# Optimization experiments

Hardware: AMD Instinct MI355X
Metric: run time of the kernel (lower is better)

The kernel has to match this reference:

```python
import jax, jax.numpy as jnp
import numpy as np

N = 50000
E = 800000
IN_DIM = 128
HID = 128
HEADS = 8
OUT_DIM = 64
LRELU_SLOPE = 0.2


def setup_inputs() -> dict:
    key = jax.random.key(0)
    ks = jax.random.split(key, 10)
    x = jax.random.normal(ks[0], (N, IN_DIM), dtype=jnp.float32)
    edge_index = jax.random.randint(ks[1], (2, E), 0, N, dtype=jnp.int64)
    c1 = HID // HEADS  # 16
    W1 = jax.random.normal(ks[2], (IN_DIM, HID), dtype=jnp.float32) * (1.0 / np.sqrt(IN_DIM))
    as1 = jax.random.normal(ks[3], (HEADS, c1), dtype=jnp.float32) * 0.1
    ad1 = jax.random.normal(ks[4], (HEADS, c1), dtype=jnp.float32) * 0.1
    b1 = jnp.zeros((HID,), dtype=jnp.float32)
    W2 = jax.random.normal(ks[5], (HID, OUT_DIM), dtype=jnp.float32) * (1.0 / np.sqrt(HID))
    as2 = jax.random.normal(ks[6], (1, OUT_DIM), dtype=jnp.float32) * 0.1
    ad2 = jax.random.normal(ks[7], (1, OUT_DIM), dtype=jnp.float32) * 0.1
    b2 = jnp.zeros((OUT_DIM,), dtype=jnp.float32)
    return {"x": x, "edge_index": edge_index, "W1": W1, "as1": as1, "ad1": ad1,
            "b1": b1, "W2": W2, "as2": as2, "ad2": ad2, "b2": b2}


def gat_conv(x, src, dst, W, a_src, a_dst, b, heads, ch, concat):
    n = x.shape[0]
    h = (x @ W).reshape(n, heads, ch)               # [N,H,C]
    alpha_s = jnp.sum(h * a_src, axis=-1)           # [N,H]
    alpha_d = jnp.sum(h * a_dst, axis=-1)           # [N,H]
    e = jax.nn.leaky_relu(alpha_s[src] + alpha_d[dst], LRELU_SLOPE)  # [E,H]
    m = jax.ops.segment_max(e, dst, num_segments=n)  # per-dst max (self-loops guarantee nonempty)
    e = jnp.exp(e - m[dst])
    denom = jax.ops.segment_sum(e, dst, num_segments=n)
    alpha = e / (denom[dst] + 1e-16)                # [E,H]
    msg = h[src] * alpha[:, :, None]                # [E,H,C]
    out = jax.ops.segment_sum(msg, dst, num_segments=n)  # [N,H,C]
    out = out.reshape(n, heads * ch) if concat else out.mean(axis=1)
    return out + b


def reference(x, edge_index, W1, as1, ad1, b1, W2, as2, ad2, b2):
    n = x.shape[0]
    loops = jnp.arange(n, dtype=edge_index.dtype)
    src = jnp.concatenate([edge_index[0], loops])   # PyG GATConv adds self-loops
    dst = jnp.concatenate([edge_index[1], loops])
    # layer 1: GATBlock (dropout is identity at eval), heads=8, concat, ELU
    h = gat_conv(x, src, dst, W1, as1, ad1, b1, HEADS, HID // HEADS, True)
    h = jax.nn.elu(h)
    # final conv: heads=1, concat=False
    out = gat_conv(h, src, dst, W2, as2, ad2, b2, 1, OUT_DIM, False)
    return jax.nn.log_softmax(out, axis=1)
```

## Files before the change

kernel.cpp:

```cpp
#include <hip/hip_runtime.h>
#include <hip/hip_bf16.h>
#include <math.h>

#define IN_DIM 128
#define HID 128
#define HEADS 8
#define OUT_DIM 64
#define SLOPE 0.2f
#define BSHIFT 7
#define BCAP 4096
#define BCAPSHIFT 12
#define EPT 8

typedef short bf16x8 __attribute__((ext_vector_type(8)));
typedef float f32x4 __attribute__((ext_vector_type(4)));

__device__ __forceinline__ float lrelu(float x) { return fmaxf(x, SLOPE * x); }
__device__ __forceinline__ float bf2f(unsigned u) { return __uint_as_float(u << 16); }
__device__ __forceinline__ unsigned short f2bf(float f) {
    unsigned u = __float_as_uint(f);
    return (unsigned short)((u + 0x7FFF + ((u >> 16) & 1)) >> 16);
}

__global__ __launch_bounds__(256) void setup_kernel(
    const float* __restrict__ W1, const float* __restrict__ W2,
    short* __restrict__ w1t, short* __restrict__ w2t, int* __restrict__ gcursor) {
    int t = threadIdx.x;
    int b = blockIdx.x;
    if (b == 96) {
        for (int i = t; i < 512; i += 256) gcursor[i] = 0;
        return;
    }
    if (b < 64) {
        int id = b * 256 + t;
        int n = id >> 7, k = id & 127;
        w1t[id] = (short)f2bf(W1[k * 128 + n]);
    } else {
        int id = (b - 64) * 256 + t;
        int n = id >> 7, k = id & 127;
        w2t[id] = (short)f2bf(W2[k * 64 + n]);
    }
}

__device__ __forceinline__ void bscatter_body(
    int blk, int* smem, const int* __restrict__ idx,
    int* __restrict__ gcursor, unsigned* __restrict__ bucket_buf,
    int E, int N, int NB) {
    int* hist  = smem;
    int* gbase = smem + 512;
    int* lbase = smem + 1024;
    int* wtot  = smem + 1536;
    int* misc  = smem + 1540;
    unsigned* sent = (unsigned*)(smem + 1552);
    unsigned* spos = (unsigned*)(smem + 3600);
    int t = threadIdx.x;
    for (int i = t; i < 512; i += 256) hist[i] = 0;
    if (t == 0) misc[1] = 0;
    __syncthreads();
    {
        int nz = (idx[2 * t + 1] != 0) + (idx[2 * t + 513] != 0);
        if (nz) atomicAdd(&misc[1], nz);
    }
    __syncthreads();
    int flag = (misc[1] > 16) ? 1 : 0;
    int e0 = blk * (256 * EPT);
    int EN = E + N;
    unsigned ent[EPT];
    int bid[EPT];
    int loc[EPT];
#pragma unroll
    for (int k = 0; k < EPT; k++) {
        int e = e0 + k * 256 + t;
        bid[k] = -1;
        if (e < EN) {
            int src, dst;
            if (e < E) {
                if (flag) { src = idx[e]; dst = idx[E + e]; }
                else      { src = idx[2 * e]; dst = idx[2 * (E + e)]; }
            } else {
                src = dst = e - E;
            }
            int b = dst >> BSHIFT;
            bid[k] = b;
            ent[k] = ((unsigned)(dst & ((1 << BSHIFT) - 1)) << 16) | (unsigned)src;
            loc[k] = atomicAdd(&hist[b], 1);
        }
    }
    __syncthreads();
    int i0 = 2 * t;
    int a = hist[i0], b2 = hist[i0 + 1];
    int ps = a + b2;
    int lane = t & 63, w = t >> 6;
    int incl = ps;
#pragma unroll
    for (int off = 1; off < 64; off <<= 1) {
        int u = __shfl_up(incl, off, 64);
        if (lane >= off) incl += u;
    }
    if (lane == 63) wtot[w] = incl;
    __syncthreads();
    int woff = 0;
    for (int k = 0; k < w; k++) woff += wtot[k];
    int ex0 = woff + incl - ps;
    lbase[i0] = ex0;
    lbase[i0 + 1] = ex0 + a;
    if (t == 255) misc[0] = woff + incl;
    for (int i = t; i < 512; i += 256) {
        int c = hist[i];
        gbase[i] = c ? atomicAdd(&gcursor[i], c) : 0;
    }
    __syncthreads();
#pragma unroll
    for (int k = 0; k < EPT; k++) {
        if (bid[k] >= 0) {
            int p = lbase[bid[k]] + loc[k];
            int pib = gbase[bid[k]] + loc[k];
            sent[p] = ent[k];
            spos[p] = (pib < BCAP) ? (((unsigned)bid[k] << BCAPSHIFT) | (unsigned)pib)
                                   : 0xFFFFFFFFu;
        }
    }
    __syncthreads();
    int tot = misc[0];
    for (int i = t; i < tot; i += 256) {
        unsigned sp = spos[i];
        if (sp != 0xFFFFFFFFu) bucket_buf[sp] = sent[i];
    }
}

__device__ __forceinline__ void gemm1_body(
    int blk, char* smemraw, const float* __restrict__ x, const short* __restrict__ w1t,
    const float* __restrict__ a_s, const float* __restrict__ a_d,
    unsigned short* __restrict__ h1g, unsigned short* __restrict__ asb,
    float* __restrict__ ad_n, int N) {
    short* Wt = (short*)smemraw;
    float* hT = (float*)smemraw;
    int t = threadIdx.x;
    const uint4* src = (const uint4*)w1t;
    for (int id = t; id < 128 * 16; id += 256) {
        int n = id >> 4, kg = id & 15;
        *(uint4*)&Wt[n * 128 + ((kg * 8) ^ ((n & 7) << 3))] = src[id];
    }
    __syncthreads();
    int wv = t >> 6, lane = t & 63;
    int m = lane & 15, q = lane >> 4;
    int row = blk * 64 + wv * 16 + m;
    f32x4 acc[8];
#pragma unroll
    for (int j = 0; j < 8; j++) acc[j] = (f32x4){0.f, 0.f, 0.f, 0.f};
    int msw = (m & 7) << 3;
#pragma unroll
    for (int k0 = 0; k0 < 128; k0 += 32) {
        bf16x8 a = {0, 0, 0, 0, 0, 0, 0, 0};
        if (row < N) {
            const float* xp = &x[(size_t)row * 128 + k0 + q * 8];
            float4 u0 = *(const float4*)xp;
            float4 u1 = *(const float4*)(xp + 4);
            a[0] = (short)f2bf(u0.x); a[1] = (short)f2bf(u0.y);
            a[2] = (short)f2bf(u0.z); a[3] = (short)f2bf(u0.w);
            a[4] = (short)f2bf(u1.x); a[5] = (short)f2bf(u1.y);
            a[6] = (short)f2bf(u1.z); a[7] = (short)f2bf(u1.w);
        }
#pragma unroll
        for (int j = 0; j < 8; j++) {
            bf16x8 b = *(const bf16x8*)&Wt[(j * 16 + m) * 128 + ((k0 + q * 8) ^ msw)];
            acc[j] = __builtin_amdgcn_mfma_f32_16x16x32_bf16(a, b, acc[j], 0, 0, 0);
        }
    }
    __syncthreads();
#pragma unroll
    for (int r = 0; r < 4; r++) {
        int rl = wv * 16 + q * 4 + r;
        int sw = ((rl >> 2) & 1) << 4;
        int rb = rl * 128;
#pragma unroll
        for (int j = 0; j < 8; j++)
            hT[rb + ((j * 16 + m) ^ sw)] = acc[j][r];
    }
    __syncthreads();
    int base = blk * 64;
    for (int id = t; id < 1024; id += 256) {
        int rl = id >> 4, c8 = (id & 15) * 8;
        int rg = base + rl;
        if (rg >= N) continue;
        int sw = ((rl >> 2) & 1) << 4;
        float4 u0 = *(const float4*)&hT[rl * 128 + (c8 ^ sw)];
        float4 u1 = *(const float4*)&hT[rl * 128 + ((c8 + 4) ^ sw)];
        uint4 ow;
        ow.x = (unsigned)f2bf(u0.x) | ((unsigned)f2bf(u0.y) << 16);
        ow.y = (unsigned)f2bf(u0.z) | ((unsigned)f2bf(u0.w) << 16);
        ow.z = (unsigned)f2bf(u1.x) | ((unsigned)f2bf(u1.y) << 16);
        ow.w = (unsigned)f2bf(u1.z) | ((unsigned)f2bf(u1.w) << 16);
        *(uint4*)&h1g[(size_t)rg * 128 + c8] = ow;
    }
    for (int it = t; it < 512; it += 256) {
        int rl = it >> 3, hd = it & 7;
        int rg = base + rl;
        int sw = ((rl >> 2) & 1) << 4;
        const float* ap = a_s + hd * 16;
        const float* dp = a_d + hd * 16;
        float s = 0.f, d = 0.f;
#pragma unroll
        for (int p = 0; p < 4; p++) {
            float4 u = *(const float4*)&hT[rl * 128 + ((hd * 16 + p * 4) ^ sw)];
            s += u.x * ap[p * 4] + u.y * ap[p * 4 + 1] + u.z * ap[p * 4 + 2] + u.w * ap[p * 4 + 3];
            d += u.x * dp[p * 4] + u.y * dp[p * 4 + 1] + u.z * dp[p * 4 + 2] + u.w * dp[p * 4 + 3];
        }
        if (rg < N) {
            asb[(size_t)base * 8 + it] = f2bf(s);
            ad_n[(size_t)base * 8 + it] = d;
        }
    }
}

__global__ __launch_bounds__(256) void k1_kernel(
    const int* __restrict__ idx, int* __restrict__ gcursor,
    unsigned* __restrict__ bucket_buf,
    const float* __restrict__ x, const short* __restrict__ w1t,
    const float* __restrict__ a_s, const float* __restrict__ a_d,
    unsigned short* __restrict__ h1g, unsigned short* __restrict__ asb,
    float* __restrict__ ad_n, int E, int N, int NB, int GS) {
    __shared__ long long smem[4096];
    if ((int)blockIdx.x < GS)
        bscatter_body(blockIdx.x, (int*)smem, idx, gcursor, bucket_buf, E, N, NB);
    else
        gemm1_body(blockIdx.x - GS, (char*)smem, x, w1t, a_s, a_d, h1g, asb, ad_n, N);
}

__device__ __forceinline__ void bsort_body(
    int b, const int* __restrict__ gcursor, const unsigned* __restrict__ bucket_buf,
    int* __restrict__ row_start, int* __restrict__ sorted_src, int N, int NB) {
    __shared__ int cnt[128];
    __shared__ int cur[128];
    __shared__ int red[4];
    __shared__ int s_w0;
    __shared__ int srt[BCAP];
    int t = threadIdx.x;
    if (t < 128) cnt[t] = 0;
    int partial = 0;
    for (int i = t; i < b; i += 256) partial += min(gcursor[i], BCAP);
#pragma unroll
    for (int msk = 32; msk > 0; msk >>= 1) partial += __shfl_xor(partial, msk, 64);
    if ((t & 63) == 0) red[t >> 6] = partial;
    __syncthreads();
    int bbase = red[0] + red[1] + red[2] + red[3];
    int c = min(gcursor[b], BCAP);
    const unsigned* buf = bucket_buf + ((size_t)b << BCAPSHIFT);
    for (int i = t; i < c; i += 256)
        atomicAdd(&cnt[(buf[i] >> 16) & 127], 1);
    __syncthreads();
    int v = (t < 128) ? cnt[t] : 0;
    int lane = t & 63;
    int incl = v;
#pragma unroll
    for (int off = 1; off < 64; off <<= 1) {
        int u = __shfl_up(incl, off, 64);
        if (lane >= off) incl += u;
    }
    if (t == 63) s_w0 = incl;
    __syncthreads();
    if (t < 128) {
        int excl = incl - v + ((t >= 64) ? s_w0 : 0);
        cur[t] = excl;
        int node = (b << BSHIFT) + t;
        if (node <= N) row_start[node] = bbase + excl;
    }
    __syncthreads();
    for (int i = t; i < c; i += 256) {
        unsigned e = buf[i];
        int lp = atomicAdd(&cur[(e >> 16) & 127], 1);
        srt[lp] = (int)(e & 0xFFFFu);
    }
    __syncthreads();
    for (int i = t; i < c; i += 256)
        sorted_src[bbase + i] = srt[i];
}

__global__ __launch_bounds__(256) void k2_kernel(
    const int* __restrict__ gcursor, const unsigned* __restrict__ bucket_buf,
    int* __restrict__ row_start, int* __restrict__ sorted_src,
    int N, int NB, int EN) {
    if (blockIdx.x == 0 && threadIdx.x < 16) sorted_src[EN + threadIdx.x] = 0;
    bsort_body(blockIdx.x, gcursor, bucket_buf, row_start, sorted_src, N, NB);
}

__global__ __launch_bounds__(256) void mid_kernel(
    const int* __restrict__ row_start, const int* __restrict__ sorted_src,
    const unsigned short* __restrict__ asb, const float* __restrict__ ad_n,
    const unsigned short* __restrict__ h1g, const float* __restrict__ b1,
    const short* __restrict__ w2t, const float* __restrict__ a_s2,
    const float* __restrict__ a_d2, unsigned short* __restrict__ h2g,
    float* __restrict__ as2n, float* __restrict__ ad2n, int N) {
    __shared__ short hA[64 * 128];
    __shared__ short Wt[64 * 136];
    int t = threadIdx.x;
    const uint4* srcw = (const uint4*)w2t;
    for (int id = t; id < 64 * 16; id += 256) {
        int n = id >> 4, kg = id & 15;
        *(uint4*)&Wt[n * 136 + kg * 8] = srcw[id];
    }
    int lane = t & 63;
    int g = lane >> 4, j = lane & 15;
    int base = blockIdx.x * 64;
    int grp16 = (t >> 6) * 4 + g;
    int e4 = j >> 2;
    int hh = (j & 3) * 2;
    int hd = j >> 1;
    int hsel = hd & 1;
    int wsrc = hd >> 1;
    for (int ni = 0; ni < 4; ni++) {
        int rowl = ni * 16 + grp16;
        int node = base + rowl;
        float acc[8];
#pragma unroll
        for (int k = 0; k < 8; k++) acc[k] = 0.f;
        float denom = 0.f;
        if (node < N) {
            float2 adp = *(const float2*)&ad_n[(size_t)node * 8 + hh];
            int beg = row_start[node], end = row_start[node + 1];
            for (int i = beg; i < end; i += 4) {
                int se = sorted_src[i + e4];
                unsigned au = *(const unsigned*)&asb[(size_t)se * 8 + hh];
                float w0 = __expf(lrelu(bf2f(au & 0xffffu) + adp.x));
                float w1 = __expf(lrelu(bf2f(au >> 16) + adp.y));
                bool val = (i + e4 < end);
                w0 = val ? w0 : 0.f;
                w1 = val ? w1 : 0.f;
#pragma unroll
                for (int e = 0; e < 4; e++) {
                    int sl = e * 4 + wsrc;
                    int sg = __shfl(se, sl, 16);
                    float wa = __shfl(w0, sl, 16);
                    float wb = __shfl(w1, sl, 16);
                    float wv = hsel ? wb : wa;
                    uint4 hv = *(const uint4*)&h1g[(size_t)sg * 128 + j * 8];
                    acc[0] += wv * bf2f(hv.x & 0xffffu);
                    acc[1] += wv * bf2f(hv.x >> 16);
                    acc[2] += wv * bf2f(hv.y & 0xffffu);
                    acc[3] += wv * bf2f(hv.y >> 16);
                    acc[4] += wv * bf2f(hv.z & 0xffffu);
                    acc[5] += wv * bf2f(hv.z >> 16);
                    acc[6] += wv * bf2f(hv.w & 0xffffu);
                    acc[7] += wv * bf2f(hv.w >> 16);
                    denom += wv;
                }
            }
        }
        float inv = 1.f / (denom + 1e-16f);
        int c0 = j * 8;
        unsigned ow[4];
#pragma unroll
        for (int p = 0; p < 4; p++) {
            float v0 = acc[2 * p] * inv + b1[c0 + 2 * p];
            float v1 = acc[2 * p + 1] * inv + b1[c0 + 2 * p + 1];
            v0 = (v0 > 0.f) ? v0 : (__expf(v0) - 1.f);
            v1 = (v1 > 0.f) ? v1 : (__expf(v1) - 1.f);
            ow[p] = (unsigned)f2bf(v0) | ((unsigned)f2bf(v1) << 16);
        }
        uint4 val = (node < N) ? make_uint4(ow[0], ow[1], ow[2], ow[3])
                               : make_uint4(0, 0, 0, 0);
        *(uint4*)&hA[rowl * 128 + ((j * 8) ^ ((rowl & 7) << 3))] = val;
    }
    __syncthreads();
    int wv = t >> 6;
    int m = lane & 15, q = lane >> 4;
    int rowl = wv * 16 + m;
    int rsw = (rowl & 7) << 3;
    f32x4 acc2[4];
#pragma unroll
    for (int j4 = 0; j4 < 4; j4++) acc2[j4] = (f32x4){0.f, 0.f, 0.f, 0.f};
#pragma unroll
    for (int k0 = 0; k0 < 128; k0 += 32) {
        bf16x8 a = *(const bf16x8*)&hA[rowl * 128 + ((k0 + q * 8) ^ rsw)];
#pragma unroll
        for (int j4 = 0; j4 < 4; j4++) {
            bf16x8 b = *(const bf16x8*)&Wt[(j4 * 16 + m) * 136 + k0 + q * 8];
            acc2[j4] = __builtin_amdgcn_mfma_f32_16x16x32_bf16(a, b, acc2[j4], 0, 0, 0);
        }
    }
    float asl[4], adl[4];
#pragma unroll
    for (int j4 = 0; j4 < 4; j4++) { asl[j4] = a_s2[j4 * 16 + m]; adl[j4] = a_d2[j4 * 16 + m]; }
    int rbase = base + wv * 16 + q * 4;
#pragma unroll
    for (int r = 0; r < 4; r++) {
        int rr = rbase + r;
        float s = 0.f, d = 0.f;
#pragma unroll
        for (int j4 = 0; j4 < 4; j4++) {
            s += acc2[j4][r] * asl[j4];
            d += acc2[j4][r] * adl[j4];
        }
#pragma unroll
        for (int msk = 8; msk > 0; msk >>= 1) {
            s += __shfl_xor(s, msk, 64);
            d += __shfl_xor(d, msk, 64);
        }
        if (rr < N) {
            if (m == 0) { as2n[rr] = s; ad2n[rr] = d; }
#pragma unroll
            for (int j4 = 0; j4 < 4; j4++)
                h2g[(size_t)rr * 64 + j4 * 16 + m] = f2bf(acc2[j4][r]);
        }
    }
}

__global__ __launch_bounds__(256) void agg2_kernel(
    const int* __restrict__ row_start, const int* __restrict__ sorted_src,
    const float* __restrict__ as_n, const float* __restrict__ ad_n,
    const unsigned short* __restrict__ h2g, const float* __restrict__ b2,
    float* __restrict__ out, int N) {
    int lane = threadIdx.x & 63;
    int g = lane >> 4, j = lane & 15;
    int node = blockIdx.x * 16 + (threadIdx.x >> 6) * 4 + g;
    if (node >= N) return;
    int e4 = j >> 2;
    float adv = ad_n[node];
    int beg = row_start[node], end = row_start[node + 1];
    float acc[4];
#pragma unroll
    for (int k = 0; k < 4; k++) acc[k] = 0.f;
    float denom = 0.f;
    for (int i = beg; i < end; i += 4) {
        int se = sorted_src[i + e4];
        float w = __expf(lrelu(as_n[se] + adv));
        w = (i + e4 < end) ? w : 0.f;
#pragma unroll
        for (int e = 0; e < 4; e++) {
            int sg = __shfl(se, e * 4, 16);
            float wvv = __shfl(w, e * 4, 16);
            uint2 hv = *(const uint2*)&h2g[(size_t)sg * 64 + j * 4];
            acc[0] += wvv * bf2f(hv.x & 0xffffu);
            acc[1] += wvv * bf2f(hv.x >> 16);
            acc[2] += wvv * bf2f(hv.y & 0xffffu);
            acc[3] += wvv * bf2f(hv.y >> 16);
            denom += wvv;
        }
    }
    float inv = 1.f / (denom + 1e-16f);
    int c0 = j * 4;
    float v[4];
#pragma unroll
    for (int k = 0; k < 4; k++) v[k] = acc[k] * inv + b2[c0 + k];
    float mx = fmaxf(fmaxf(v[0], v[1]), fmaxf(v[2], v[3]));
#pragma unroll
    for (int msk = 8; msk > 0; msk >>= 1) mx = fmaxf(mx, __shfl_xor(mx, msk, 64));
    float ex = __expf(v[0] - mx) + __expf(v[1] - mx) + __expf(v[2] - mx) + __expf(v[3] - mx);
#pragma unroll
    for (int msk = 8; msk > 0; msk >>= 1) ex += __shfl_xor(ex, msk, 64);
    float lse = mx + __logf(ex);
    *(float4*)&out[(size_t)node * 64 + c0] = make_float4(v[0] - lse, v[1] - lse, v[2] - lse, v[3] - lse);
}

extern "C" void kernel_launch(void* const* d_in, const int* in_sizes, int n_in,
                              void* d_out, int out_size, void* d_ws, size_t ws_size,
                              hipStream_t stream) {
    const float* x   = (const float*)d_in[0];
    const int*   idx = (const int*)d_in[1];
    const float* W1  = (const float*)d_in[2];
    const float* as1 = (const float*)d_in[3];
    const float* ad1 = (const float*)d_in[4];
    const float* b1  = (const float*)d_in[5];
    const float* W2  = (const float*)d_in[6];
    const float* as2 = (const float*)d_in[7];
    const float* ad2 = (const float*)d_in[8];
    const float* b2  = (const float*)d_in[9];
    float* out = (float*)d_out;

    const int N = in_sizes[0] / IN_DIM;
    const int E = in_sizes[1] / 2;
    const int EN = E + N;
    const int NB = (N + (1 << BSHIFT) - 1) >> BSHIFT;
    const int GS = (EN + 256 * EPT - 1) / (256 * EPT);
    const int T1 = (N + 63) / 64;

    unsigned short* h1g   = (unsigned short*)d_ws;
    unsigned short* h1act = h1g + (size_t)N * 128;
    unsigned short* h2g   = h1act + (size_t)N * 128;
    unsigned short* as1b  = (unsigned short*)(h2g + (size_t)N * 64);
    float* ad1n = (float*)(as1b + (size_t)N * 8) + (size_t)N * 4;
    float* as2n = ad1n + (size_t)N * 8;
    float* ad2n = as2n + (size_t)N;
    int* row_start  = (int*)(ad2n + (size_t)N);
    int* gcursor    = row_start + N + 1;
    unsigned* bucket_buf = (unsigned*)(gcursor + 512);
    int* sorted_src = (int*)(bucket_buf + ((size_t)NB << BCAPSHIFT));
    short* w1t = (short*)((((uintptr_t)(sorted_src + EN + 16)) + 15) & ~(uintptr_t)15);
    short* w2t = w1t + 128 * 128;
    (void)ws_size; (void)n_in; (void)out_size;

    setup_kernel<<<97, 256, 0, stream>>>(W1, W2, w1t, w2t, gcursor);
    k1_kernel<<<GS + T1, 256, 0, stream>>>(idx, gcursor, bucket_buf,
                                           x, w1t, as1, ad1, h1g, as1b, ad1n, E, N, NB, GS);
    k2_kernel<<<NB, 256, 0, stream>>>(gcursor, bucket_buf, row_start, sorted_src, N, NB, EN);
    mid_kernel<<<T1, 256, 0, stream>>>(row_start, sorted_src, as1b, ad1n, h1g, b1,
                                       w2t, as2, ad2, h2g, as2n, ad2n, N);
    agg2_kernel<<<(N + 15) / 16, 256, 0, stream>>>(row_start, sorted_src, as2n, ad2n, h2g, b2, out, N);
}
```

Measured before the change: 183.3 us.

## Halve mid_kernel nodes per block and split GEMM columns across waves

The fused layer-1 aggregation plus layer-2 projection kernel now handles 32 nodes per block instead of 64, doubling the grid. In the MFMA stage each wave computes one row tile of 16 and half of the 64 output columns. The two attention-logit partial sums per row are combined through shared memory after an extra barrier. The goal is more blocks for better occupancy and load balance across CUs during the irregular gather phase, at the cost of reloading W2 into LDS twice as often and an additional sync.

```diff
diff --git a/kernel.cpp b/kernel.cpp
--- a/kernel.cpp
+++ b/kernel.cpp
@@ -291,8 +291,10 @@
     const short* __restrict__ w2t, const float* __restrict__ a_s2,
     const float* __restrict__ a_d2, unsigned short* __restrict__ h2g,
     float* __restrict__ as2n, float* __restrict__ ad2n, int N) {
-    __shared__ short hA[64 * 128];
+    __shared__ short hA[32 * 128];
     __shared__ short Wt[64 * 136];
+    __shared__ float sP[2][32];
+    __shared__ float dP[2][32];
     int t = threadIdx.x;
     const uint4* srcw = (const uint4*)w2t;
     for (int id = t; id < 64 * 16; id += 256) {
@@ -301,14 +303,14 @@
     }
     int lane = t & 63;
     int g = lane >> 4, j = lane & 15;
-    int base = blockIdx.x * 64;
+    int base = blockIdx.x * 32;
     int grp16 = (t >> 6) * 4 + g;
     int e4 = j >> 2;
     int hh = (j & 3) * 2;
     int hd = j >> 1;
     int hsel = hd & 1;
     int wsrc = hd >> 1;
-    for (int ni = 0; ni < 4; ni++) {
+    for (int ni = 0; ni < 2; ni++) {
         int rowl = ni * 16 + grp16;
         int node = base + rowl;
         float acc[8];
@@ -363,33 +365,40 @@
     }
     __syncthreads();
     int wv = t >> 6;
+    int rt = wv & 1;
+    int cp = wv >> 1;
     int m = lane & 15, q = lane >> 4;
-    int rowl = wv * 16 + m;
+    int rowl = rt * 16 + m;
     int rsw = (rowl & 7) << 3;
-    f32x4 acc2[4];
-#pragma unroll
-    for (int j4 = 0; j4 < 4; j4++) acc2[j4] = (f32x4){0.f, 0.f, 0.f, 0.f};
+    f32x4 acc2[2];
+#pragma unroll
+    for (int jj = 0; jj < 2; jj++) acc2[jj] = (f32x4){0.f, 0.f, 0.f, 0.f};
 #pragma unroll
     for (int k0 = 0; k0 < 128; k0 += 32) {
         bf16x8 a = *(const bf16x8*)&hA[rowl * 128 + ((k0 + q * 8) ^ rsw)];
 #pragma unroll
-        for (int j4 = 0; j4 < 4; j4++) {
+        for (int jj = 0; jj < 2; jj++) {
+            int j4 = cp * 2 + jj;
             bf16x8 b = *(const bf16x8*)&Wt[(j4 * 16 + m) * 136 + k0 + q * 8];
-            acc2[j4] = __builtin_amdgcn_mfma_f32_16x16x32_bf16(a, b, acc2[j4], 0, 0, 0);
-        }
-    }
-    float asl[4], adl[4];
-#pragma unroll
-    for (int j4 = 0; j4 < 4; j4++) { asl[j4] = a_s2[j4 * 16 + m]; adl[j4] = a_d2[j4 * 16 + m]; }
-    int rbase = base + wv * 16 + q * 4;
+            acc2[jj] = __builtin_amdgcn_mfma_f32_16x16x32_bf16(a, b, acc2[jj], 0, 0, 0);
+        }
+    }
+    float asl[2], adl[2];
+#pragma unroll
+    for (int jj = 0; jj < 2; jj++) {
+        asl[jj] = a_s2[(cp * 2 + jj) * 16 + m];
+        adl[jj] = a_d2[(cp * 2 + jj) * 16 + m];
+    }
+    int rb = rt * 16 + q * 4;
 #pragma unroll
     for (int r = 0; r < 4; r++) {
-        int rr = rbase + r;
+        int rl2 = rb + r;
+        int rr = base + rl2;
         float s = 0.f, d = 0.f;
 #pragma unroll
-        for (int j4 = 0; j4 < 4; j4++) {
-            s += acc2[j4][r] * asl[j4];
-            d += acc2[j4][r] * adl[j4];
+        for (int jj = 0; jj < 2; jj++) {
+            s += acc2[jj][r] * asl[jj];
+            d += acc2[jj][r] * adl[jj];
         }
 #pragma unroll
         for (int msk = 8; msk > 0; msk >>= 1) {
@@ -397,10 +406,18 @@
             d += __shfl_xor(d, msk, 64);
         }
         if (rr < N) {
-            if (m == 0) { as2n[rr] = s; ad2n[rr] = d; }
-#pragma unroll
-            for (int j4 = 0; j4 < 4; j4++)
-                h2g[(size_t)rr * 64 + j4 * 16 + m] = f2bf(acc2[j4][r]);
+            if (m == 0) { sP[cp][rl2] = s; dP[cp][rl2] = d; }
+#pragma unroll
+            for (int jj = 0; jj < 2; jj++)
+                h2g[(size_t)rr * 64 + (cp * 2 + jj) * 16 + m] = f2bf(acc2[jj][r]);
+        }
+    }
+    __syncthreads();
+    if (t < 32) {
+        int rr = base + t;
+        if (rr < N) {
+            as2n[rr] = sP[0][t] + sP[1][t];
+            ad2n[rr] = dP[0][t] + dP[1][t];
         }
     }
 }
@@ -473,6 +490,7 @@
     const int NB = (N + (1 << BSHIFT) - 1) >> BSHIFT;
     const int GS = (EN + 256 * EPT - 1) / (256 * EPT);
     const int T1 = (N + 63) / 64;
+    const int T2 = (N + 31) / 32;
 
     unsigned short* h1g   = (unsigned short*)d_ws;
     unsigned short* h1act = h1g + (size_t)N * 128;
@@ -493,7 +511,7 @@
     k1_kernel<<<GS + T1, 256, 0, stream>>>(idx, gcursor, bucket_buf,
                                            x, w1t, as1, ad1, h1g, as1b, ad1n, E, N, NB, GS);
     k2_kernel<<<NB, 256, 0, stream>>>(gcursor, bucket_buf, row_start, sorted_src, N, NB, EN);
-    mid_kernel<<<T1, 256, 0, stream>>>(row_start, sorted_src, as1b, ad1n, h1g, b1,
+    mid_kernel<<<T2, 256, 0, stream>>>(row_start, sorted_src, as1b, ad1n, h1g, b1,
                                        w2t, as2, ad2, h2g, as2n, ad2n, N);
     agg2_kernel<<<(N + 15) / 16, 256, 0, stream>>>(row_start, sorted_src, as2n, ad2n, h2g, b2, out, N);
 }
```

Result: no change. 186.9 us (+2.0%).
